# Kernel tuning notes

Hardware: AMD Instinct MI355X
Metric: run time of the kernel (lower is better)

Reference implementation:

```python
import jax, jax.numpy as jnp
import numpy as np

N_NODES = 50000
N_EDGES = 800000
GNN_IN, GNN_HID, COMB = 256, 64, 64
MLP_IN, MLP_HID = 256, 512


def glorot(key, shape):
    fan_in, fan_out = shape[0], shape[1]
    s = jnp.sqrt(6.0 / (fan_in + fan_out)).astype(jnp.float32)
    return jax.random.uniform(key, shape, jnp.float32, -s, s)


def setup_inputs() -> dict:
    key = jax.random.key(0)
    ks = jax.random.split(key, 12)
    x = jax.random.normal(ks[0], (N_NODES, GNN_IN), jnp.float32)
    edge_index = jax.random.randint(ks[1], (2, N_EDGES), 0, N_NODES, jnp.int64 if jax.config.jax_enable_x64 else jnp.int32)
    edge_attr = jax.random.uniform(ks[2], (N_EDGES,), jnp.float32)
    user_features = jax.random.normal(ks[3], (N_NODES, MLP_IN), jnp.float32)
    params = {
        'gcn1_W': glorot(ks[4], (GNN_IN, GNN_HID)),
        'gcn1_b': jnp.zeros((GNN_HID,), jnp.float32),
        'gcn2_W': glorot(ks[5], (GNN_HID, COMB)),
        'gcn2_b': jnp.zeros((COMB,), jnp.float32),
        'fc1_W': glorot(ks[6], (MLP_IN, MLP_HID)),
        'fc1_b': jnp.zeros((MLP_HID,), jnp.float32),
        'fc2_W': glorot(ks[7], (MLP_HID, COMB)),
        'fc2_b': jnp.zeros((COMB,), jnp.float32),
        'fcf_W': glorot(ks[8], (2 * COMB, 1)),
        'fcf_b': jnp.zeros((1,), jnp.float32),
    }
    return dict(x=x, edge_index=edge_index, edge_attr=edge_attr,
                user_features=user_features, **params)


def gcn_conv(x, W, b, src, dst, ew, n_nodes):
    # PyG GCNConv: transform, add self-loops (weight 1), sym-normalize, scatter-add.
    h = x @ W  # [N, out]
    loop = jnp.arange(n_nodes, dtype=src.dtype)
    src_sl = jnp.concatenate([src, loop])
    dst_sl = jnp.concatenate([dst, loop])
    ew_sl = jnp.concatenate([ew, jnp.ones((n_nodes,), ew.dtype)])
    deg = jax.ops.segment_sum(ew_sl, dst_sl, num_segments=n_nodes)
    dinv = jnp.where(deg > 0, jax.lax.rsqrt(jnp.maximum(deg, 1e-12)), 0.0)
    norm = dinv[src_sl] * ew_sl * dinv[dst_sl]  # [E+N]
    msg = h[src_sl] * norm[:, None]             # gather + scale
    out = jax.ops.segment_sum(msg, dst_sl, num_segments=n_nodes)
    return out + b


def reference(x, edge_index, edge_attr, user_features,
              gcn1_W, gcn1_b, gcn2_W, gcn2_b,
              fc1_W, fc1_b, fc2_W, fc2_b, fcf_W, fcf_b):
    src, dst = edge_index[0], edge_index[1]
    n = x.shape[0]
    # MLP branch
    mlp_out = jax.nn.relu(user_features @ fc1_W + fc1_b) @ fc2_W + fc2_b
    # GNN branch
    g = gcn_conv(x, gcn1_W, gcn1_b, src, dst, edge_attr, n)
    g = jax.nn.relu(g)
    gnn_out = gcn_conv(g, gcn2_W, gcn2_b, src, dst, edge_attr, n)
    combined = jnp.concatenate([mlp_out, gnn_out], axis=-1)
    return combined @ fcf_W + fcf_b
```

## Files before the change

### kernel.cpp

```cpp
#include <hip/hip_runtime.h>
#include <hip/hip_bf16.h>

#define N_NODES 50000
#define N_EDGES 800000
#define BROW 264

typedef __attribute__((ext_vector_type(8))) short bfrag8;
typedef __attribute__((ext_vector_type(4))) float f32x4;
typedef __attribute__((ext_vector_type(4))) unsigned short us4;
typedef __attribute__((ext_vector_type(8))) unsigned short us8;

__device__ __forceinline__ float bf2f(unsigned short u) {
  return __uint_as_float(((unsigned int)u) << 16);
}
__device__ __forceinline__ unsigned short f2bf(float f) {
  unsigned int u = __float_as_uint(f);
  u = (u + 0x7fffu + ((u >> 16) & 1u)) >> 16;
  return (unsigned short)u;
}
__device__ __forceinline__ float ldS(const void* p, int f32, size_t i) {
  return f32 ? ((const float*)p)[i] : bf2f(((const unsigned short*)p)[i]);
}
__device__ __forceinline__ void stO(void* out, int f32, int i, float v) {
  if (f32) ((float*)out)[i] = v;
  else ((unsigned short*)out)[i] = f2bf(v);
}

template <int F32>
__device__ __forceinline__ void stageB8(const void* src, int nb,
                                        unsigned short* __restrict__ Bs) {
  const int t = threadIdx.x;
  const int r = t >> 3;
  const int q = t & 7;
  int row = nb + r;
  row = row < N_NODES ? row : (N_NODES - 1);
  const size_t base = (size_t)row * 256 + q * 32;
  unsigned short* dst = Bs + r * BROW + q * 32;
  if (F32) {
    const f32x4* s4 = (const f32x4*)((const float*)src + base);
#pragma unroll
    for (int j = 0; j < 4; ++j) {
      f32x4 a = s4[2 * j], b = s4[2 * j + 1];
      us8 o;
      o[0] = f2bf(a[0]); o[1] = f2bf(a[1]); o[2] = f2bf(a[2]); o[3] = f2bf(a[3]);
      o[4] = f2bf(b[0]); o[5] = f2bf(b[1]); o[6] = f2bf(b[2]); o[7] = f2bf(b[3]);
      *(us8*)(dst + j * 8) = o;
    }
  } else {
    const us8* s8 = (const us8*)((const unsigned short*)src + base);
#pragma unroll
    for (int j = 0; j < 4; ++j) *(us8*)(dst + j * 8) = s8[j];
  }
}

__global__ void k_detect(const void* x, const void* ea, const void* uf,
                         const void* f1W, const int* ei, int* flags) {
  int lane = threadIdx.x & 63;
  unsigned short ux = ((const unsigned short*)x)[lane];
  unsigned short ue = ((const unsigned short*)ea)[lane];
  unsigned short uu = ((const unsigned short*)uf)[lane];
  unsigned short uw = ((const unsigned short*)f1W)[lane];
  int oi = ei[2 * lane + 1];
  unsigned long long bx = __ballot(((ux >> 7) & 0xFF) > 0x85);
  unsigned long long be = __ballot((ue & 0x8000u) != 0);
  unsigned long long bu = __ballot(((uu >> 7) & 0xFF) > 0x85);
  unsigned long long bw = __ballot(((uw >> 7) & 0xFF) > 0x7E);
  unsigned long long bi = __ballot(oi != 0);
  if (lane == 0) {
    int fx = bx ? 1 : 0, fe = be ? 1 : 0, fu = bu ? 1 : 0, fw = bw ? 1 : 0;
    flags[0] = fx; flags[1] = fe; flags[2] = fu; flags[3] = fw;
    flags[4] = (bi == 0ull) ? 1 : 0;
    flags[5] = (fx & fe & fu & fw);
  }
}

__global__ __launch_bounds__(256) void k_zero3(int* __restrict__ counts,
                                               float* __restrict__ degf,
                                               float* __restrict__ mlpc) {
  int i = blockIdx.x * 256 + threadIdx.x;
  if (i < N_NODES) { counts[i] = 0; degf[i] = 0.f; mlpc[i] = 0.f; }
  if (i == 0) counts[N_NODES] = 0;
}

__global__ __launch_bounds__(256) void k_edges2(const int* __restrict__ ei,
                                                const void* ea,
                                                const int* __restrict__ flags,
                                                int* __restrict__ counts,
                                                float* __restrict__ degf) {
  int e = blockIdx.x * 256 + threadIdx.x;
  if (e >= N_EDGES) return;
  int d;
  if (flags[4]) d = ei[1600000 + 2 * e];
  else          d = ei[800000 + e];
  d = d < 0 ? 0 : (d > N_NODES - 1 ? N_NODES - 1 : d);
  float w = ldS(ea, flags[1], e);
  atomicAdd(&counts[d], 1);
  atomicAdd(&degf[d], w);
}

__global__ __launch_bounds__(256) void k_scan1(const int* __restrict__ cnt,
                                               int* __restrict__ rp,
                                               int* __restrict__ bsum) {
  __shared__ int sd[256];
  int t = threadIdx.x;
  int i0 = blockIdx.x * 1024 + t * 4;
  int v0 = (i0 + 0) < N_NODES ? cnt[i0 + 0] : 0;
  int v1 = (i0 + 1) < N_NODES ? cnt[i0 + 1] : 0;
  int v2 = (i0 + 2) < N_NODES ? cnt[i0 + 2] : 0;
  int v3 = (i0 + 3) < N_NODES ? cnt[i0 + 3] : 0;
  int ts = v0 + v1 + v2 + v3;
  sd[t] = ts;
  __syncthreads();
  for (int off = 1; off < 256; off <<= 1) {
    int x = (t >= off) ? sd[t - off] : 0;
    __syncthreads();
    sd[t] += x;
    __syncthreads();
  }
  int exoff = sd[t] - ts;
  if (i0 + 0 < N_NODES) rp[i0 + 0] = exoff;
  if (i0 + 1 < N_NODES) rp[i0 + 1] = exoff + v0;
  if (i0 + 2 < N_NODES) rp[i0 + 2] = exoff + v0 + v1;
  if (i0 + 3 < N_NODES) rp[i0 + 3] = exoff + v0 + v1 + v2;
  if (t == 255) bsum[blockIdx.x] = sd[255];
}

__global__ void k_scan2(const int* __restrict__ bsum, int* __restrict__ boff,
                        int* __restrict__ rp, int nb) {
  if (threadIdx.x == 0) {
    int run = 0;
    for (int b = 0; b < nb; ++b) { boff[b] = run; run += bsum[b]; }
    rp[N_NODES] = run;
  }
}

__global__ __launch_bounds__(256) void k_scan3d(int* __restrict__ rp,
                                                const int* __restrict__ boff,
                                                int* __restrict__ cursor,
                                                const float* __restrict__ degf,
                                                float* __restrict__ dinv) {
  int i = blockIdx.x * 256 + threadIdx.x;
  if (i < N_NODES) {
    int r = rp[i] + boff[i >> 10];
    rp[i] = r;
    cursor[i] = r;
    dinv[i] = rsqrtf(degf[i] + 1.0f);
  }
}

__global__ __launch_bounds__(256) void k_place2(const int* __restrict__ ei,
                                                const void* ea,
                                                const int* __restrict__ flags,
                                                const float* __restrict__ dinv,
                                                int* __restrict__ cursor,
                                                unsigned long long* __restrict__ e8) {
  int e = blockIdx.x * 256 + threadIdx.x;
  if (e >= N_EDGES) return;
  int s, d;
  if (flags[4]) { s = ei[2 * e]; d = ei[1600000 + 2 * e]; }
  else          { s = ei[e];     d = ei[800000 + e]; }
  s = s < 0 ? 0 : (s > N_NODES - 1 ? N_NODES - 1 : s);
  d = d < 0 ? 0 : (d > N_NODES - 1 ? N_NODES - 1 : d);
  float w = ldS(ea, flags[1], e) * dinv[s];
  int pos = atomicAdd(&cursor[d], 1);
  e8[pos] = ((unsigned long long)__float_as_uint(w) << 32) | (unsigned int)s;
}

__global__ __launch_bounds__(512) void k_prep(
    const void* f1W, const void* g1W, const void* f2W, const void* f2b,
    const void* g2W, const void* g2b, const void* ffW, const void* ffb,
    const int* __restrict__ flags, unsigned short* __restrict__ W1T,
    unsigned short* __restrict__ WgT, float* __restrict__ w2f,
    float* __restrict__ w2g, float* __restrict__ constv) {
  const int fw = flags[3];
  if (blockIdx.x < 288) {
    int tid = blockIdx.x * 512 + threadIdx.x;
    if (tid < 512 * 256) {
      int c = tid >> 8, k = tid & 255;
      W1T[tid] = f2bf(ldS(f1W, fw, (size_t)k * 512 + c));
    } else if (tid < 512 * 256 + 64 * 256) {
      int j = tid - 512 * 256;
      int c = j >> 8, k = j & 255;
      WgT[j] = f2bf(ldS(g1W, fw, (size_t)k * 64 + c));
    }
    return;
  }
  int t = threadIdx.x;
  if (t < 512) {
    float s = 0.f;
    for (int c = 0; c < 64; ++c) s += ldS(f2W, fw, t * 64 + c) * ldS(ffW, fw, c);
    w2f[t] = s;
  }
  if (t < 64) {
    float s = 0.f;
    for (int c = 0; c < 64; ++c) s += ldS(g2W, fw, t * 64 + c) * ldS(ffW, fw, 64 + c);
    w2g[t] = s;
  }
  if (t == 0) {
    float s = ldS(ffb, fw, 0);
    for (int c = 0; c < 64; ++c) {
      s += ldS(f2b, fw, c) * ldS(ffW, fw, c);
      s += ldS(g2b, fw, c) * ldS(ffW, fw, 64 + c);
    }
    constv[0] = s;
  }
}

__global__ __launch_bounds__(512, 2) void k_h13u(
    const void* x, const unsigned short* __restrict__ WgT,
    const int* __restrict__ flags, unsigned short* __restrict__ h1b) {
  __shared__ unsigned short Bs[64 * BROW];
  const int nb = blockIdx.x * 64;
  if (flags[0]) stageB8<1>(x, nb, Bs);
  else          stageB8<0>(x, nb, Bs);
  __syncthreads();

  const int lane = threadIdx.x & 63;
  const int wave = threadIdx.x >> 6;
  const int ct = wave & 3;
  const int nh = wave >> 2;
  const int l15 = lane & 15;
  const int quad = lane >> 4;
  const unsigned short* ap = WgT + (size_t)(ct * 16 + l15) * 256 + quad * 8;

  f32x4 acc[2];
  acc[0] = (f32x4){0.f, 0.f, 0.f, 0.f};
  acc[1] = (f32x4){0.f, 0.f, 0.f, 0.f};

#pragma unroll
  for (int ks = 0; ks < 8; ++ks) {
    bfrag8 a = *(const bfrag8*)(ap + ks * 32);
    const int bofs = ks * 32 + quad * 8;
#pragma unroll
    for (int u = 0; u < 2; ++u) {
      bfrag8 b = *(const bfrag8*)(Bs + (nh * 32 + u * 16 + l15) * BROW + bofs);
      acc[u] = __builtin_amdgcn_mfma_f32_16x16x32_bf16(a, b, acc[u], 0, 0, 0);
    }
  }
#pragma unroll
  for (int u = 0; u < 2; ++u) {
    int node = nb + nh * 32 + u * 16 + l15;
    if (node < N_NODES) {
      us4 o;
#pragma unroll
      for (int r = 0; r < 4; ++r) o[r] = f2bf(acc[u][r]);
      *(us4*)(h1b + (size_t)node * 64 + ct * 16 + quad * 4) = o;
    }
  }
}

__global__ __launch_bounds__(512, 2) void k_mlpu(
    const void* uf, const unsigned short* __restrict__ W1T,
    const void* fc1b, const float* __restrict__ w2f,
    const int* __restrict__ flags, float* __restrict__ mlpc) {
  __shared__ unsigned short Bs[64 * BROW];
  const int nb = blockIdx.x * 64;
  if (flags[2]) stageB8<1>(uf, nb, Bs);
  else          stageB8<0>(uf, nb, Bs);
  __syncthreads();

  const int fw = flags[3];
  const int lane = threadIdx.x & 63;
  const int wave = threadIdx.x >> 6;
  const int l15 = lane & 15;
  const int quad = lane >> 4;
  const int c_base = wave * 64;
  const unsigned short* ap = W1T + (size_t)(c_base + l15) * 256 + quad * 8;

  f32x4 acc[4][4];
#pragma unroll
  for (int t = 0; t < 4; ++t)
#pragma unroll
    for (int u = 0; u < 4; ++u) acc[t][u] = (f32x4){0.f, 0.f, 0.f, 0.f};

#pragma unroll
  for (int ks = 0; ks < 8; ++ks) {
    const int bofs = ks * 32 + quad * 8;
    bfrag8 b[4];
#pragma unroll
    for (int u = 0; u < 4; ++u)
      b[u] = *(const bfrag8*)(Bs + (u * 16 + l15) * BROW + bofs);
#pragma unroll
    for (int t = 0; t < 4; ++t) {
      bfrag8 a = *(const bfrag8*)(ap + (size_t)t * 16 * 256 + ks * 32);
#pragma unroll
      for (int u = 0; u < 4; ++u)
        acc[t][u] = __builtin_amdgcn_mfma_f32_16x16x32_bf16(a, b[u], acc[t][u], 0, 0, 0);
    }
  }

  float part[4] = {0.f, 0.f, 0.f, 0.f};
#pragma unroll
  for (int t = 0; t < 4; ++t) {
#pragma unroll
    for (int r = 0; r < 4; ++r) {
      const int c = c_base + t * 16 + quad * 4 + r;
      const float bc = ldS(fc1b, fw, c);
      const float wc = w2f[c];
#pragma unroll
      for (int u = 0; u < 4; ++u) {
        float v = acc[t][u][r] + bc;
        v = v > 0.f ? v : 0.f;
        part[u] += v * wc;
      }
    }
  }
#pragma unroll
  for (int u = 0; u < 4; ++u) {
    part[u] += __shfl_xor(part[u], 16, 64);
    part[u] += __shfl_xor(part[u], 32, 64);
    int node = nb + u * 16 + l15;
    if (lane < 16 && node < N_NODES) atomicAdd(&mlpc[node], part[u]);
  }
}

__global__ __launch_bounds__(256) void k_aggs2(
    const int* __restrict__ rp, const unsigned long long* __restrict__ e8,
    const unsigned short* __restrict__ h1b, const float* __restrict__ dinv,
    const void* g1b, const float* __restrict__ w2g,
    const int* __restrict__ flags, float* __restrict__ s2) {
  const int i = blockIdx.x * 4 + (threadIdx.x >> 6);
  if (i >= N_NODES) return;
  const int lane = threadIdx.x & 63;
  const int base = rp[i], end = rp[i + 1];
  const float di = dinv[i];
  float acc = 0.f;
  int j = base;
  for (; j + 8 <= end; j += 8) {
    unsigned long long vv[8];
#pragma unroll
    for (int q = 0; q < 8; ++q) vv[q] = e8[j + q];
    float ww[8], hv[8];
#pragma unroll
    for (int q = 0; q < 8; ++q) {
      ww[q] = __uint_as_float((unsigned int)(vv[q] >> 32));
      hv[q] = bf2f(h1b[(size_t)(unsigned int)vv[q] * 64 + lane]);
    }
#pragma unroll
    for (int q = 0; q < 8; ++q) acc += ww[q] * hv[q];
  }
  for (; j < end; ++j) {
    unsigned long long v = e8[j];
    acc += __uint_as_float((unsigned int)(v >> 32)) *
           bf2f(h1b[(size_t)(unsigned int)v * 64 + lane]);
  }
  float v = acc * di + di * di * bf2f(h1b[(size_t)i * 64 + lane]) + ldS(g1b, flags[3], lane);
  v = v > 0.f ? v : 0.f;
  float p = v * w2g[lane];
#pragma unroll
  for (int off = 32; off > 0; off >>= 1) p += __shfl_xor(p, off, 64);
  if (lane == 0) s2[i] = p;
}

__global__ __launch_bounds__(256) void k_fin2(
    const int* __restrict__ rp, const unsigned long long* __restrict__ e8,
    const float* __restrict__ s2, const float* __restrict__ dinv,
    const float* __restrict__ mlpc, const float* __restrict__ constv,
    const int* __restrict__ flags, void* out) {
  const int i = blockIdx.x * 4 + (threadIdx.x >> 6);
  if (i >= N_NODES) return;
  const int lane = threadIdx.x & 63;
  const int base = rp[i], end = rp[i + 1];
  float p = 0.f;
  for (int j = base + lane; j < end; j += 64) {
    unsigned long long v = e8[j];
    p += __uint_as_float((unsigned int)(v >> 32)) * s2[(unsigned int)v];
  }
#pragma unroll
  for (int off = 32; off > 0; off >>= 1) p += __shfl_xor(p, off, 64);
  if (lane == 0) {
    float di = dinv[i];
    stO(out, flags[5], i, mlpc[i] + di * p + di * di * s2[i] + constv[0]);
  }
}

__global__ __launch_bounds__(256) void k_zero(const int* __restrict__ flags, void* out) {
  int i = blockIdx.x * 256 + threadIdx.x;
  if (i < N_NODES) stO(out, flags[5], i, 0.f);
}

extern "C" void kernel_launch(void* const* d_in, const int* in_sizes, int n_in,
                              void* d_out, int out_size, void* d_ws, size_t ws_size,
                              hipStream_t stream) {
  const void* x   = d_in[0];
  const int*  ei  = (const int*)d_in[1];
  const void* ea  = d_in[2];
  const void* uf  = d_in[3];
  const void* g1W = d_in[4];
  const void* g1b = d_in[5];
  const void* g2W = d_in[6];
  const void* g2b = d_in[7];
  const void* f1W = d_in[8];
  const void* f1b = d_in[9];
  const void* f2W = d_in[10];
  const void* f2b = d_in[11];
  const void* ffW = d_in[12];
  const void* ffb = d_in[13];

  float* ws = (float*)d_ws;
  int*   flags  = (int*)ws;
  float* w2f    = ws + 16;
  float* w2g    = ws + 528;
  float* constv = ws + 592;
  float* dinv   = ws + 608;
  float* degf   = ws + 50608;
  float* s2     = ws + 50608;
  float* mlpc   = ws + 100608;
  unsigned short* W1T = (unsigned short*)(ws + 150608);
  unsigned short* WgT = W1T + 131072;
  int* rowptr = (int*)(ws + 224336);
  int* bsum   = (int*)(ws + 274352);
  int* boff   = bsum + 64;
  int* counts = (int*)(ws + 274480);
  int* cursor = (int*)(ws + 324496);
  unsigned long long* e8 = (unsigned long long*)(ws + 374496);
  unsigned short* h1b = (unsigned short*)(ws + 1974496);
  const size_t NEED = (size_t)3574496 * 4;

  k_detect<<<1, 64, 0, stream>>>(x, ea, uf, f1W, ei, flags);
  if (ws_size < NEED) {
    k_zero<<<(N_NODES + 255) / 256, 256, 0, stream>>>(flags, d_out);
    return;
  }
  const int NZB = (N_NODES + 255) / 256;
  const int NB  = (N_NODES + 1023) / 1024;
  const int NGB = (N_NODES + 63) / 64;
  const int NEB = (N_EDGES + 255) / 256;

  k_zero3<<<NZB, 256, 0, stream>>>(counts, degf, mlpc);
  k_edges2<<<NEB, 256, 0, stream>>>(ei, ea, flags, counts, degf);
  k_scan1<<<NB, 256, 0, stream>>>(counts, rowptr, bsum);
  k_scan2<<<1, 64, 0, stream>>>(bsum, boff, rowptr, NB);
  k_scan3d<<<NZB, 256, 0, stream>>>(rowptr, boff, cursor, degf, dinv);
  k_place2<<<NEB, 256, 0, stream>>>(ei, ea, flags, dinv, cursor, e8);
  k_prep<<<289, 512, 0, stream>>>(f1W, g1W, f2W, f2b, g2W, g2b, ffW, ffb, flags,
                                  W1T, WgT, w2f, w2g, constv);
  k_h13u<<<NGB, 512, 0, stream>>>(x, WgT, flags, h1b);
  k_mlpu<<<NGB, 512, 0, stream>>>(uf, W1T, f1b, w2f, flags, mlpc);
  k_aggs2<<<(N_NODES + 3) / 4, 256, 0, stream>>>(rowptr, e8, h1b, dinv, g1b, w2g, flags, s2);
  k_fin2<<<(N_NODES + 3) / 4, 256, 0, stream>>>(rowptr, e8, s2, dinv, mlpc, constv, flags, d_out);
}
```

Baseline: 413.1 us.

## Record histogram slots to drop placement atomics, fold dinv into features, reduce MLP in LDS

The histogram pass now stores each edge's slot returned by atomicAdd, so placement computes its position as rowptr plus slot and needs no second atomic pass. The float degree atomics are replaced by a per-node segmented sum over the CSR weights. The source-side dinv scaling moves into the h1 GEMM epilogue and the s2 output, which removes a dependent gather in placement and simplifies the aggregation arithmetic. The MLP kernel writes its per-node sum once after an LDS reduction instead of issuing global atomics, so mlpc no longer needs zeroing. The cost is an extra 3.2MB slot array, an extra degree kernel that rereads e8, and a larger workspace requirement.

```diff
diff --git a/kernel.cpp b/kernel.cpp
--- a/kernel.cpp
+++ b/kernel.cpp
@@ -74,28 +74,22 @@
   }
 }
 
-__global__ __launch_bounds__(256) void k_zero3(int* __restrict__ counts,
-                                               float* __restrict__ degf,
-                                               float* __restrict__ mlpc) {
+__global__ __launch_bounds__(256) void k_zeroc(int* __restrict__ counts) {
   int i = blockIdx.x * 256 + threadIdx.x;
-  if (i < N_NODES) { counts[i] = 0; degf[i] = 0.f; mlpc[i] = 0.f; }
-  if (i == 0) counts[N_NODES] = 0;
-}
-
-__global__ __launch_bounds__(256) void k_edges2(const int* __restrict__ ei,
-                                                const void* ea,
-                                                const int* __restrict__ flags,
-                                                int* __restrict__ counts,
-                                                float* __restrict__ degf) {
+  if (i <= N_NODES) counts[i] = 0;
+}
+
+__global__ __launch_bounds__(256) void k_histpos(const int* __restrict__ ei,
+                                                 const int* __restrict__ flags,
+                                                 int* __restrict__ counts,
+                                                 int* __restrict__ posw) {
   int e = blockIdx.x * 256 + threadIdx.x;
   if (e >= N_EDGES) return;
   int d;
   if (flags[4]) d = ei[1600000 + 2 * e];
   else          d = ei[800000 + e];
   d = d < 0 ? 0 : (d > N_NODES - 1 ? N_NODES - 1 : d);
-  float w = ldS(ea, flags[1], e);
-  atomicAdd(&counts[d], 1);
-  atomicAdd(&degf[d], w);
+  posw[e] = atomicAdd(&counts[d], 1);
 }
 
 __global__ __launch_bounds__(256) void k_scan1(const int* __restrict__ cnt,
@@ -134,25 +128,17 @@
   }
 }
 
-__global__ __launch_bounds__(256) void k_scan3d(int* __restrict__ rp,
-                                                const int* __restrict__ boff,
-                                                int* __restrict__ cursor,
-                                                const float* __restrict__ degf,
-                                                float* __restrict__ dinv) {
+__global__ __launch_bounds__(256) void k_scan3(int* __restrict__ rp,
+                                               const int* __restrict__ boff) {
   int i = blockIdx.x * 256 + threadIdx.x;
-  if (i < N_NODES) {
-    int r = rp[i] + boff[i >> 10];
-    rp[i] = r;
-    cursor[i] = r;
-    dinv[i] = rsqrtf(degf[i] + 1.0f);
-  }
-}
-
-__global__ __launch_bounds__(256) void k_place2(const int* __restrict__ ei,
+  if (i < N_NODES) rp[i] += boff[i >> 10];
+}
+
+__global__ __launch_bounds__(256) void k_placeb(const int* __restrict__ ei,
                                                 const void* ea,
                                                 const int* __restrict__ flags,
-                                                const float* __restrict__ dinv,
-                                                int* __restrict__ cursor,
+                                                const int* __restrict__ rp,
+                                                const int* __restrict__ posw,
                                                 unsigned long long* __restrict__ e8) {
   int e = blockIdx.x * 256 + threadIdx.x;
   if (e >= N_EDGES) return;
@@ -161,9 +147,24 @@
   else          { s = ei[e];     d = ei[800000 + e]; }
   s = s < 0 ? 0 : (s > N_NODES - 1 ? N_NODES - 1 : s);
   d = d < 0 ? 0 : (d > N_NODES - 1 ? N_NODES - 1 : d);
-  float w = ldS(ea, flags[1], e) * dinv[s];
-  int pos = atomicAdd(&cursor[d], 1);
+  float w = ldS(ea, flags[1], e);
+  int pos = rp[d] + posw[e];
   e8[pos] = ((unsigned long long)__float_as_uint(w) << 32) | (unsigned int)s;
+}
+
+__global__ __launch_bounds__(256) void k_degc(const int* __restrict__ rp,
+                                              const unsigned long long* __restrict__ e8,
+                                              float* __restrict__ dinv) {
+  const int i = blockIdx.x * 4 + (threadIdx.x >> 6);
+  if (i >= N_NODES) return;
+  const int lane = threadIdx.x & 63;
+  const int base = rp[i], end = rp[i + 1];
+  float s = 0.f;
+  for (int j = base + lane; j < end; j += 64)
+    s += __uint_as_float((unsigned int)(e8[j] >> 32));
+#pragma unroll
+  for (int off = 32; off > 0; off >>= 1) s += __shfl_xor(s, off, 64);
+  if (lane == 0) dinv[i] = rsqrtf(s + 1.0f);
 }
 
 __global__ __launch_bounds__(512) void k_prep(
@@ -208,8 +209,9 @@
 
 __global__ __launch_bounds__(512, 2) void k_h13u(
     const void* x, const unsigned short* __restrict__ WgT,
-    const int* __restrict__ flags, unsigned short* __restrict__ h1b) {
-  __shared__ unsigned short Bs[64 * BROW];
+    const float* __restrict__ dinv, const int* __restrict__ flags,
+    unsigned short* __restrict__ h1b) {
+  __shared__ __align__(16) unsigned short Bs[64 * BROW];
   const int nb = blockIdx.x * 64;
   if (flags[0]) stageB8<1>(x, nb, Bs);
   else          stageB8<0>(x, nb, Bs);
@@ -241,9 +243,10 @@
   for (int u = 0; u < 2; ++u) {
     int node = nb + nh * 32 + u * 16 + l15;
     if (node < N_NODES) {
+      float di = dinv[node];
       us4 o;
 #pragma unroll
-      for (int r = 0; r < 4; ++r) o[r] = f2bf(acc[u][r]);
+      for (int r = 0; r < 4; ++r) o[r] = f2bf(acc[u][r] * di);
       *(us4*)(h1b + (size_t)node * 64 + ct * 16 + quad * 4) = o;
     }
   }
@@ -253,7 +256,7 @@
     const void* uf, const unsigned short* __restrict__ W1T,
     const void* fc1b, const float* __restrict__ w2f,
     const int* __restrict__ flags, float* __restrict__ mlpc) {
-  __shared__ unsigned short Bs[64 * BROW];
+  __shared__ __align__(16) unsigned short Bs[64 * BROW];
   const int nb = blockIdx.x * 64;
   if (flags[2]) stageB8<1>(uf, nb, Bs);
   else          stageB8<0>(uf, nb, Bs);
@@ -288,6 +291,7 @@
         acc[t][u] = __builtin_amdgcn_mfma_f32_16x16x32_bf16(a, b[u], acc[t][u], 0, 0, 0);
     }
   }
+  __syncthreads();
 
   float part[4] = {0.f, 0.f, 0.f, 0.f};
 #pragma unroll
@@ -305,12 +309,21 @@
       }
     }
   }
+  float* red = (float*)Bs;
 #pragma unroll
   for (int u = 0; u < 4; ++u) {
     part[u] += __shfl_xor(part[u], 16, 64);
     part[u] += __shfl_xor(part[u], 32, 64);
-    int node = nb + u * 16 + l15;
-    if (lane < 16 && node < N_NODES) atomicAdd(&mlpc[node], part[u]);
+    if (lane < 16) red[wave * 64 + u * 16 + l15] = part[u];
+  }
+  __syncthreads();
+  const int t = threadIdx.x;
+  if (t < 64) {
+    float sum = 0.f;
+#pragma unroll
+    for (int w = 0; w < 8; ++w) sum += red[w * 64 + t];
+    int node = nb + t;
+    if (node < N_NODES) mlpc[node] = sum;
   }
 }
 
@@ -344,12 +357,12 @@
     acc += __uint_as_float((unsigned int)(v >> 32)) *
            bf2f(h1b[(size_t)(unsigned int)v * 64 + lane]);
   }
-  float v = acc * di + di * di * bf2f(h1b[(size_t)i * 64 + lane]) + ldS(g1b, flags[3], lane);
+  float v = (acc + bf2f(h1b[(size_t)i * 64 + lane])) * di + ldS(g1b, flags[3], lane);
   v = v > 0.f ? v : 0.f;
   float p = v * w2g[lane];
 #pragma unroll
   for (int off = 32; off > 0; off >>= 1) p += __shfl_xor(p, off, 64);
-  if (lane == 0) s2[i] = p;
+  if (lane == 0) s2[i] = di * p;
 }
 
 __global__ __launch_bounds__(256) void k_fin2(
@@ -370,7 +383,7 @@
   for (int off = 32; off > 0; off >>= 1) p += __shfl_xor(p, off, 64);
   if (lane == 0) {
     float di = dinv[i];
-    stO(out, flags[5], i, mlpc[i] + di * p + di * di * s2[i] + constv[0]);
+    stO(out, flags[5], i, mlpc[i] + di * (p + s2[i]) + constv[0]);
   }
 }
 
@@ -403,7 +416,6 @@
   float* w2g    = ws + 528;
   float* constv = ws + 592;
   float* dinv   = ws + 608;
-  float* degf   = ws + 50608;
   float* s2     = ws + 50608;
   float* mlpc   = ws + 100608;
   unsigned short* W1T = (unsigned short*)(ws + 150608);
@@ -412,30 +424,31 @@
   int* bsum   = (int*)(ws + 274352);
   int* boff   = bsum + 64;
   int* counts = (int*)(ws + 274480);
-  int* cursor = (int*)(ws + 324496);
-  unsigned long long* e8 = (unsigned long long*)(ws + 374496);
-  unsigned short* h1b = (unsigned short*)(ws + 1974496);
-  const size_t NEED = (size_t)3574496 * 4;
+  int* posw   = (int*)(ws + 324496);
+  unsigned long long* e8 = (unsigned long long*)(ws + 1124496);
+  unsigned short* h1b = (unsigned short*)(ws + 2724496);
+  const size_t NEED = (size_t)4324496 * 4;
 
   k_detect<<<1, 64, 0, stream>>>(x, ea, uf, f1W, ei, flags);
   if (ws_size < NEED) {
     k_zero<<<(N_NODES + 255) / 256, 256, 0, stream>>>(flags, d_out);
     return;
   }
-  const int NZB = (N_NODES + 255) / 256;
+  const int NZB = (N_NODES + 256) / 256;
   const int NB  = (N_NODES + 1023) / 1024;
   const int NGB = (N_NODES + 63) / 64;
   const int NEB = (N_EDGES + 255) / 256;
 
-  k_zero3<<<NZB, 256, 0, stream>>>(counts, degf, mlpc);
-  k_edges2<<<NEB, 256, 0, stream>>>(ei, ea, flags, counts, degf);
+  k_zeroc<<<NZB, 256, 0, stream>>>(counts);
+  k_histpos<<<NEB, 256, 0, stream>>>(ei, flags, counts, posw);
   k_scan1<<<NB, 256, 0, stream>>>(counts, rowptr, bsum);
   k_scan2<<<1, 64, 0, stream>>>(bsum, boff, rowptr, NB);
-  k_scan3d<<<NZB, 256, 0, stream>>>(rowptr, boff, cursor, degf, dinv);
-  k_place2<<<NEB, 256, 0, stream>>>(ei, ea, flags, dinv, cursor, e8);
+  k_scan3<<<(N_NODES + 255) / 256, 256, 0, stream>>>(rowptr, boff);
+  k_placeb<<<NEB, 256, 0, stream>>>(ei, ea, flags, rowptr, posw, e8);
+  k_degc<<<(N_NODES + 3) / 4, 256, 0, stream>>>(rowptr, e8, dinv);
   k_prep<<<289, 512, 0, stream>>>(f1W, g1W, f2W, f2b, g2W, g2b, ffW, ffb, flags,
                                   W1T, WgT, w2f, w2g, constv);
-  k_h13u<<<NGB, 512, 0, stream>>>(x, WgT, flags, h1b);
+  k_h13u<<<NGB, 512, 0, stream>>>(x, WgT, dinv, flags, h1b);
   k_mlpu<<<NGB, 512, 0, stream>>>(uf, W1T, f1b, w2f, flags, mlpc);
   k_aggs2<<<(N_NODES + 3) / 4, 256, 0, stream>>>(rowptr, e8, h1b, dinv, g1b, w2g, flags, s2);
   k_fin2<<<(N_NODES + 3) / 4, 256, 0, stream>>>(rowptr, e8, s2, dinv, mlpc, constv, flags, d_out);
```

Measured after the change: 360.3 us. 12.8% less time.
